# Optimization experiments

Hardware: AMD Instinct MI355X
Metric: run time of the kernel (lower is better)

Reference implementation:

```python
import jax, jax.numpy as jnp
import numpy as np

N_NODES = 50000
N_EDGES = 600000
DIM = 128
HEADS = 8
HEAD_DIM = DIM // HEADS  # 16


def leaky(x, slope=0.01):
    return jnp.where(x >= 0, x, slope * x)


def gat_layer(x, W, a_src, a_dst, bias, src, dst):
    # x: [N, DIM]; W: [DIM, DIM]; a_src/a_dst: [HEADS, HEAD_DIM]; bias: [DIM]
    N = x.shape[0]
    xh = (x @ W).reshape(N, HEADS, HEAD_DIM)
    alpha_src = jnp.sum(xh * a_src, axis=-1)  # [N, H]
    alpha_dst = jnp.sum(xh * a_dst, axis=-1)  # [N, H]
    e = leaky(alpha_src[src] + alpha_dst[dst], 0.2)  # [E, H], PyG negative_slope=0.2
    # segment softmax over edges sharing the same destination node
    e_max = jax.ops.segment_max(e, dst, num_segments=N)
    ex = jnp.exp(e - e_max[dst])
    denom = jax.ops.segment_sum(ex, dst, num_segments=N)
    alpha = ex / (denom[dst] + 1e-16)
    out = jax.ops.segment_sum(xh[src] * alpha[:, :, None], dst, num_segments=N)
    return out.reshape(N, DIM) + bias


def setup_inputs() -> dict:
    key = jax.random.key(0)
    ks = jax.random.split(key, 20)
    s_d = 1.0 / np.sqrt(DIM)
    s_h = 1.0 / np.sqrt(DIM // 2)
    inp = {
        'features': jax.random.normal(ks[0], (N_NODES, DIM), jnp.float32),
        'edge_index': jax.random.randint(ks[1], (2, N_EDGES), 0, N_NODES, jnp.int64)
            if jax.config.jax_enable_x64 else
            jax.random.randint(ks[1], (2, N_EDGES), 0, N_NODES).astype(jnp.int32),
        'W1': jax.random.normal(ks[2], (DIM, DIM), jnp.float32) * s_d,
        'a_src1': jax.random.normal(ks[3], (HEADS, HEAD_DIM), jnp.float32) * s_d,
        'a_dst1': jax.random.normal(ks[4], (HEADS, HEAD_DIM), jnp.float32) * s_d,
        'b1': jnp.zeros((DIM,), jnp.float32),
        'W2': jax.random.normal(ks[5], (DIM, DIM), jnp.float32) * s_d,
        'a_src2': jax.random.normal(ks[6], (HEADS, HEAD_DIM), jnp.float32) * s_d,
        'a_dst2': jax.random.normal(ks[7], (HEADS, HEAD_DIM), jnp.float32) * s_d,
        'b2': jnp.zeros((DIM,), jnp.float32),
        'wm1': jax.random.normal(ks[8], (DIM, DIM // 2), jnp.float32) * s_d,
        'bm1': jnp.zeros((DIM // 2,), jnp.float32),
        'wm2': jax.random.normal(ks[9], (DIM // 2, 1), jnp.float32) * s_h,
        'bm2': jnp.zeros((1,), jnp.float32),
        'wa1': jax.random.normal(ks[10], (DIM, DIM // 2), jnp.float32) * s_d,
        'ba1': jnp.zeros((DIM // 2,), jnp.float32),
        'wa2': jax.random.normal(ks[11], (DIM // 2, DIM), jnp.float32) * s_h,
        'ba2': jnp.zeros((DIM,), jnp.float32),
        'gamma': jnp.ones((DIM,), jnp.float32),
        'beta': jnp.zeros((DIM,), jnp.float32),
    }
    return inp


def reference(features, edge_index, W1, a_src1, a_dst1, b1, W2, a_src2, a_dst2, b2,
              wm1, bm1, wm2, bm2, wa1, ba1, wa2, ba2, gamma, beta):
    N = features.shape[0]
    loops = jnp.arange(N, dtype=edge_index.dtype)
    src = jnp.concatenate([edge_index[0], loops])  # PyG add_self_loops=True
    dst = jnp.concatenate([edge_index[1], loops])
    h = leaky(gat_layer(features, W1, a_src1, a_dst1, b1, src, dst))
    h = leaky(gat_layer(h, W2, a_src2, a_dst2, b2, src, dst))
    scores = (leaky(h @ wm1 + bm1) @ wm2 + bm2)[:, 0]  # [N]
    w = jax.nn.softmax(scores, axis=0)
    agg = jnp.sum(w[:, None] * h, axis=0)  # [DIM]
    z = leaky(agg @ wa1 + ba1) @ wa2 + ba2
    mu = jnp.mean(z)
    var = jnp.mean((z - mu) ** 2)
    return gamma * (z - mu) / jnp.sqrt(var + 1e-5) + beta
```

## Files before the change

kernel.cpp:

```cpp
#include <hip/hip_runtime.h>
#include <math.h>

#define DIM 128
#define HEADS 8
#define HD 16
#define CAP 64
#define WAGG_NB 512

typedef __attribute__((ext_vector_type(8))) short s16x8;
typedef __attribute__((ext_vector_type(8))) unsigned short u16x8;
typedef __attribute__((ext_vector_type(4))) float f32x4;

__device__ __forceinline__ float lrelu(float x, float s) { return x >= 0.f ? x : s * x; }

__device__ __forceinline__ unsigned short f2bf(float x) {
  unsigned u = __float_as_uint(x);
  return (unsigned short)((u + 0x7FFFu + ((u >> 16) & 1u)) >> 16);
}
__device__ __forceinline__ float bf2f(unsigned short b) {
  return __uint_as_float(((unsigned)b) << 16);
}

__global__ void k_hist(const int* __restrict__ ei, int E, int N, int* __restrict__ cnt) {
  int tot = E + N;
  for (int i = blockIdx.x * blockDim.x + threadIdx.x; i < tot; i += gridDim.x * blockDim.x) {
    int d = (i < E) ? ei[E + i] : (i - E);
    atomicAdd(&cnt[d], 1);
  }
}

__global__ __launch_bounds__(256) void k_scan_blk(const int* __restrict__ cnt, int n,
                                                  int* __restrict__ excl, int* __restrict__ bsum) {
  __shared__ int wsum[4];
  int tid = threadIdx.x, l = tid & 63, w = tid >> 6;
  int i = blockIdx.x * 256 + tid;
  int v = (i < n) ? cnt[i] : 0;
  int s = v;
#pragma unroll
  for (int off = 1; off < 64; off <<= 1) {
    int t = __shfl_up(s, off, 64);
    if (l >= off) s += t;
  }
  if (l == 63) wsum[w] = s;
  __syncthreads();
  int add = 0;
#pragma unroll
  for (int k = 0; k < 4; ++k) add += (k < w) ? wsum[k] : 0;
  if (i < n) excl[i] = s + add - v;
  if (tid == 255) bsum[blockIdx.x] = s + add;
}

__global__ __launch_bounds__(256) void k_scan_top(const int* __restrict__ bsum, int nb,
                                                  int* __restrict__ boff, int* __restrict__ rowptrN) {
  __shared__ int wsum[4];
  int tid = threadIdx.x, l = tid & 63, w = tid >> 6;
  int v = (tid < nb) ? bsum[tid] : 0;
  int s = v;
#pragma unroll
  for (int off = 1; off < 64; off <<= 1) {
    int t = __shfl_up(s, off, 64);
    if (l >= off) s += t;
  }
  if (l == 63) wsum[w] = s;
  __syncthreads();
  int add = 0;
#pragma unroll
  for (int k = 0; k < 4; ++k) add += (k < w) ? wsum[k] : 0;
  if (tid < nb) boff[tid] = s + add - v;
  if (tid == 255) *rowptrN = s + add;
}

__global__ __launch_bounds__(256) void k_scan_fix(int* __restrict__ cursor, const int* __restrict__ boff,
                                                  int n, int* __restrict__ rowptr) {
  int i = blockIdx.x * 256 + threadIdx.x;
  if (i < n) {
    int r = boff[blockIdx.x] + cursor[i];
    rowptr[i] = r;
    cursor[i] = r;
  }
}

__global__ void k_scatter(const int* __restrict__ ei, int E, int N,
                          int* __restrict__ cursor, int* __restrict__ colb) {
  int tot = E + N;
  for (int i = blockIdx.x * blockDim.x + threadIdx.x; i < tot; i += gridDim.x * blockDim.x) {
    int s, d;
    if (i < E) { s = ei[i]; d = ei[E + i]; } else { s = i - E; d = s; }
    int pos = atomicAdd(&cursor[d], 1);
    colb[pos] = s;
  }
}

__global__ __launch_bounds__(256) void k_prep(
    const float* __restrict__ W1, const float* __restrict__ as1, const float* __restrict__ ad1,
    const float* __restrict__ W2, const float* __restrict__ as2, const float* __restrict__ ad2,
    const float* __restrict__ wm1,
    unsigned short* __restrict__ wh1,
    unsigned short* __restrict__ sh1, unsigned short* __restrict__ sl1,
    unsigned short* __restrict__ wh2,
    unsigned short* __restrict__ sh2, unsigned short* __restrict__ sl2,
    unsigned short* __restrict__ mh, unsigned short* __restrict__ ml,
    int* __restrict__ cnt, int N) {
  int b = blockIdx.x, tid = threadIdx.x;
  if (b < 32) {
    int layer = b >> 4;
    const float* W = layer ? W2 : W1;
    unsigned short* wh = layer ? wh2 : wh1;
    int lo = (b & 15) * 1024;
    for (int idx = lo + tid; idx < lo + 1024; idx += 256) {
      int n = idx >> 7, k = idx & 127;
      wh[idx] = f2bf(W[k * DIM + n]);
    }
  } else if (b < 36) {
    int layer = (b - 32) >> 1;
    const float* W = layer ? W2 : W1;
    const float* avs = layer ? as2 : as1;
    const float* avd = layer ? ad2 : ad1;
    unsigned short* sh = layer ? sh2 : sh1;
    unsigned short* sl = layer ? sl2 : sl1;
    int lo = ((b - 32) & 1) * 1024;
    for (int idx = lo + tid; idx < lo + 1024; idx += 256) {
      int n = idx >> 7, k = idx & 127;
      float acc = 0.f;
      if (n < 8) {
#pragma unroll
        for (int j = 0; j < 16; ++j) acc += W[k * DIM + n * 16 + j] * avs[n * 16 + j];
      } else {
        int h = n - 8;
#pragma unroll
        for (int j = 0; j < 16; ++j) acc += W[k * DIM + h * 16 + j] * avd[h * 16 + j];
      }
      unsigned short hb = f2bf(acc);
      sh[idx] = hb;
      sl[idx] = f2bf(acc - bf2f(hb));
    }
  } else if (b < 44) {
    int lo = (b - 36) * 1024;
    for (int idx = lo + tid; idx < lo + 1024; idx += 256) {
      int j = idx >> 7, k = idx & 127;
      float v = wm1[k * 64 + j];
      unsigned short hb = f2bf(v);
      mh[idx] = hb;
      ml[idx] = f2bf(v - bf2f(hb));
    }
  } else {
    int i0 = (b - 44) * 2048 + tid * 8;
    if (i0 + 8 <= N) {
      int4 z = {0, 0, 0, 0};
      *(int4*)(cnt + i0) = z;
      *(int4*)(cnt + i0 + 4) = z;
    } else {
      for (int i = i0; i < N; ++i) cnt[i] = 0;
    }
  }
}

template <int BF16IN>
__global__ __launch_bounds__(256) void k_linear_mfma(
    const void* __restrict__ xin,
    const unsigned short* __restrict__ wh,
    const unsigned short* __restrict__ sh, const unsigned short* __restrict__ sl,
    unsigned short* __restrict__ xhb, float* __restrict__ asrc, float* __restrict__ adst,
    int N, int nrt) {
  int tid = threadIdx.x, l = tid & 63, w = tid >> 6;
  int g = l >> 4, c = l & 15;
  int t0 = w * 2, t1 = w * 2 + 1;

  const s16x8* Bh = (const s16x8*)wh;
  const s16x8* Shp = (const s16x8*)sh;
  const s16x8* Slp = (const s16x8*)sl;
  s16x8 B0[4], B1[4], S0[4], S1[4];
#pragma unroll
  for (int kt = 0; kt < 4; ++kt) {
    B0[kt] = Bh[(t0 * 16 + c) * 16 + kt * 4 + g];
    B1[kt] = Bh[(t1 * 16 + c) * 16 + kt * 4 + g];
    S0[kt] = Shp[c * 16 + kt * 4 + g];
    S1[kt] = Slp[c * 16 + kt * 4 + g];
  }

  for (int rt = blockIdx.x; rt < nrt; rt += gridDim.x) {
    int rbase = rt * 16;
    int rc = min(rbase + c, N - 1);
    s16x8 A[4];
    if constexpr (BF16IN) {
      const s16x8* xr = (const s16x8*)((const unsigned short*)xin + (size_t)rc * DIM);
#pragma unroll
      for (int kt = 0; kt < 4; ++kt) A[kt] = xr[kt * 4 + g];
    } else {
      const float4* xf = (const float4*)((const float*)xin + (size_t)rc * DIM);
#pragma unroll
      for (int kt = 0; kt < 4; ++kt) {
        float4 p = xf[kt * 8 + g * 2];
        float4 q = xf[kt * 8 + g * 2 + 1];
        s16x8 a;
        a[0] = (short)f2bf(p.x); a[1] = (short)f2bf(p.y);
        a[2] = (short)f2bf(p.z); a[3] = (short)f2bf(p.w);
        a[4] = (short)f2bf(q.x); a[5] = (short)f2bf(q.y);
        a[6] = (short)f2bf(q.z); a[7] = (short)f2bf(q.w);
        A[kt] = a;
      }
    }
    f32x4 acc0 = {0.f, 0.f, 0.f, 0.f}, acc1 = {0.f, 0.f, 0.f, 0.f};
#pragma unroll
    for (int kt = 0; kt < 4; ++kt) {
      acc0 = __builtin_amdgcn_mfma_f32_16x16x32_bf16(A[kt], B0[kt], acc0, 0, 0, 0);
      acc1 = __builtin_amdgcn_mfma_f32_16x16x32_bf16(A[kt], B1[kt], acc1, 0, 0, 0);
    }
#pragma unroll
    for (int r = 0; r < 4; ++r) {
      int rr = rbase + g * 4 + r;
      if (rr < N) {
        xhb[(size_t)rr * DIM + t0 * 16 + c] = f2bf(acc0[r]);
        xhb[(size_t)rr * DIM + t1 * 16 + c] = f2bf(acc1[r]);
      }
    }
    if (w == 0) {
      f32x4 accS = {0.f, 0.f, 0.f, 0.f};
#pragma unroll
      for (int kt = 0; kt < 4; ++kt) {
        accS = __builtin_amdgcn_mfma_f32_16x16x32_bf16(A[kt], S0[kt], accS, 0, 0, 0);
        accS = __builtin_amdgcn_mfma_f32_16x16x32_bf16(A[kt], S1[kt], accS, 0, 0, 0);
      }
#pragma unroll
      for (int r = 0; r < 4; ++r) {
        int rr = rbase + g * 4 + r;
        if (rr < N) {
          if (c < 8) asrc[rr * HEADS + c] = accS[r];
          else adst[rr * HEADS + (c - 8)] = accS[r];
        }
      }
    }
  }
}

__global__ __launch_bounds__(256) void k_gat_agg(const int* __restrict__ rowptr, const int* __restrict__ colb,
                                                 const unsigned short* __restrict__ xhb,
                                                 const float* __restrict__ asrc, const float* __restrict__ adst,
                                                 const float* __restrict__ bias,
                                                 unsigned short* __restrict__ houtb, int N) {
  __shared__ int ci[4][CAP];
  int tid = threadIdx.x, lane = tid & 63, wv = tid >> 6;
  int n = blockIdx.x * 4 + wv;
  int base = 0, deg = 0;
  if (n < N) { base = rowptr[n]; deg = rowptr[n + 1] - base; }
  if (lane < deg && lane < CAP) ci[wv][lane] = colb[base + lane];
  __syncthreads();
  if (n >= N) return;

  int qt = lane >> 4, q = lane & 15;
  int h = q >> 1;
  float adn = adst[n * HEADS + h];
  float den = 0.f;
  float a0 = 0.f, a1 = 0.f, a2 = 0.f, a3 = 0.f, a4 = 0.f, a5 = 0.f, a6 = 0.f, a7 = 0.f;
#define EDGE(ii) { \
    int c_ = ((ii) < CAP) ? ci[wv][(ii)] : colb[base + (ii)]; \
    float e_ = lrelu(asrc[c_ * HEADS + h] + adn, 0.2f); \
    float w_ = __expf(e_); \
    den += w_; \
    u16x8 u_ = *(const u16x8*)(xhb + (size_t)c_ * DIM + q * 8); \
    a0 = fmaf(w_, bf2f((unsigned short)u_[0]), a0); \
    a1 = fmaf(w_, bf2f((unsigned short)u_[1]), a1); \
    a2 = fmaf(w_, bf2f((unsigned short)u_[2]), a2); \
    a3 = fmaf(w_, bf2f((unsigned short)u_[3]), a3); \
    a4 = fmaf(w_, bf2f((unsigned short)u_[4]), a4); \
    a5 = fmaf(w_, bf2f((unsigned short)u_[5]), a5); \
    a6 = fmaf(w_, bf2f((unsigned short)u_[6]), a6); \
    a7 = fmaf(w_, bf2f((unsigned short)u_[7]), a7); }
  int i = qt;
  for (; i + 4 < deg; i += 8) { EDGE(i); EDGE(i + 4); }
  for (; i < deg; i += 4) { EDGE(i); }
#undef EDGE
  den += __shfl_xor(den, 16, 64); den += __shfl_xor(den, 32, 64);
  a0 += __shfl_xor(a0, 16, 64); a0 += __shfl_xor(a0, 32, 64);
  a1 += __shfl_xor(a1, 16, 64); a1 += __shfl_xor(a1, 32, 64);
  a2 += __shfl_xor(a2, 16, 64); a2 += __shfl_xor(a2, 32, 64);
  a3 += __shfl_xor(a3, 16, 64); a3 += __shfl_xor(a3, 32, 64);
  a4 += __shfl_xor(a4, 16, 64); a4 += __shfl_xor(a4, 32, 64);
  a5 += __shfl_xor(a5, 16, 64); a5 += __shfl_xor(a5, 32, 64);
  a6 += __shfl_xor(a6, 16, 64); a6 += __shfl_xor(a6, 32, 64);
  a7 += __shfl_xor(a7, 16, 64); a7 += __shfl_xor(a7, 32, 64);
  if (qt == 0) {
    float r = 1.f / (den + 1e-16f);
    const float4* bp = (const float4*)(bias + q * 8);
    float4 b0 = bp[0], b1 = bp[1];
    u16x8 o;
    o[0] = f2bf(lrelu(fmaf(a0, r, b0.x), 0.01f));
    o[1] = f2bf(lrelu(fmaf(a1, r, b0.y), 0.01f));
    o[2] = f2bf(lrelu(fmaf(a2, r, b0.z), 0.01f));
    o[3] = f2bf(lrelu(fmaf(a3, r, b0.w), 0.01f));
    o[4] = f2bf(lrelu(fmaf(a4, r, b1.x), 0.01f));
    o[5] = f2bf(lrelu(fmaf(a5, r, b1.y), 0.01f));
    o[6] = f2bf(lrelu(fmaf(a6, r, b1.z), 0.01f));
    o[7] = f2bf(lrelu(fmaf(a7, r, b1.w), 0.01f));
    *(u16x8*)(houtb + (size_t)n * DIM + q * 8) = o;
  }
}

__global__ __launch_bounds__(256) void k_score_mfma(
    const unsigned short* __restrict__ h2b,
    const unsigned short* __restrict__ mh, const unsigned short* __restrict__ ml,
    const float* __restrict__ bm1, const float* __restrict__ wm2, const float* __restrict__ bm2,
    float* __restrict__ scores, int N) {
  int tid = threadIdx.x, l = tid & 63, w = tid >> 6;
  int g = l >> 4, c = l & 15;
  int rbase = blockIdx.x * 64 + w * 16;
  int rc = min(rbase + c, N - 1);
  const s16x8* xr = (const s16x8*)(h2b + (size_t)rc * DIM);
  s16x8 A[4];
#pragma unroll
  for (int kt = 0; kt < 4; ++kt) A[kt] = xr[kt * 4 + g];

  const s16x8* Bh = (const s16x8*)mh;
  const s16x8* Bl = (const s16x8*)ml;
  float v[4] = {0.f, 0.f, 0.f, 0.f};
#pragma unroll
  for (int ct = 0; ct < 4; ++ct) {
    f32x4 acc = {0.f, 0.f, 0.f, 0.f};
#pragma unroll
    for (int kt = 0; kt < 4; ++kt) {
      s16x8 bh = Bh[(ct * 16 + c) * 16 + kt * 4 + g];
      s16x8 bl = Bl[(ct * 16 + c) * 16 + kt * 4 + g];
      acc = __builtin_amdgcn_mfma_f32_16x16x32_bf16(A[kt], bh, acc, 0, 0, 0);
      acc = __builtin_amdgcn_mfma_f32_16x16x32_bf16(A[kt], bl, acc, 0, 0, 0);
    }
    int col = ct * 16 + c;
    float b = bm1[col], w2 = wm2[col];
#pragma unroll
    for (int r = 0; r < 4; ++r) v[r] += lrelu(acc[r] + b, 0.01f) * w2;
  }
#pragma unroll
  for (int r = 0; r < 4; ++r) {
    v[r] += __shfl_xor(v[r], 1, 64);
    v[r] += __shfl_xor(v[r], 2, 64);
    v[r] += __shfl_xor(v[r], 4, 64);
    v[r] += __shfl_xor(v[r], 8, 64);
  }
  if (c == 0) {
    float b2 = bm2[0];
#pragma unroll
    for (int r = 0; r < 4; ++r) {
      int rr = rbase + g * 4 + r;
      if (rr < N) scores[rr] = v[r] + b2;
    }
  }
}

__global__ __launch_bounds__(128) void k_wagg(const float* __restrict__ scores,
                                              const unsigned short* __restrict__ h2b,
                                              int N, float* __restrict__ pagg, float* __restrict__ psum) {
  int d = threadIdx.x;
  float acc = 0.f, zs = 0.f;
  for (int n = blockIdx.x; n < N; n += gridDim.x) {
    float e = __expf(scores[n]);
    acc = fmaf(e, bf2f(h2b[(size_t)n * DIM + d]), acc);
    zs += e;
  }
  pagg[blockIdx.x * DIM + d] = acc;
  if (d == 0) psum[blockIdx.x] = zs;
}

__global__ __launch_bounds__(1024) void k_final(const float* __restrict__ psum, const float* __restrict__ pagg,
                                                int nb,
                                                const float* __restrict__ wa1, const float* __restrict__ ba1,
                                                const float* __restrict__ wa2, const float* __restrict__ ba2,
                                                const float* __restrict__ gamma, const float* __restrict__ beta,
                                                float* __restrict__ out) {
  __shared__ float redz[1024];
  __shared__ float reda[8][128];
  __shared__ float sa[128], shh[64], red[128];
  int t = threadIdx.x;
  float zp = 0.f;
  for (int b = t; b < nb; b += 1024) zp += psum[b];
  redz[t] = zp;
  __syncthreads();
  for (int st = 512; st > 0; st >>= 1) { if (t < st) redz[t] += redz[t + st]; __syncthreads(); }
  int d = t & 127, g = t >> 7;
  float ag = 0.f;
  for (int b = g; b < nb; b += 8) ag += pagg[b * DIM + d];
  reda[g][d] = ag;
  __syncthreads();
  if (g == 0) {
    float s = 0.f;
#pragma unroll
    for (int k = 0; k < 8; ++k) s += reda[k][d];
    sa[d] = s / redz[0];
  }
  __syncthreads();
  if (t < 64) {
    float a = 0.f;
    for (int k = 0; k < 128; ++k) a = fmaf(sa[k], wa1[k * 64 + t], a);
    a += ba1[t];
    shh[t] = lrelu(a, 0.01f);
  }
  __syncthreads();
  float zval = 0.f;
  if (t < 128) {
    zval = ba2[t];
    for (int j = 0; j < 64; ++j) zval = fmaf(shh[j], wa2[j * 128 + t], zval);
    red[t] = zval;
  }
  __syncthreads();
  for (int st = 64; st > 0; st >>= 1) { if (t < st) red[t] += red[t + st]; __syncthreads(); }
  float mu = red[0] / 128.f;
  __syncthreads();
  if (t < 128) red[t] = (zval - mu) * (zval - mu);
  __syncthreads();
  for (int st = 64; st > 0; st >>= 1) { if (t < st) red[t] += red[t + st]; __syncthreads(); }
  float var = red[0] / 128.f;
  if (t < 128) out[t] = gamma[t] * (zval - mu) / sqrtf(var + 1e-5f) + beta[t];
}

extern "C" void kernel_launch(void* const* d_in, const int* in_sizes, int n_in,
                              void* d_out, int out_size, void* d_ws, size_t ws_size,
                              hipStream_t stream) {
  const float* feat = (const float*)d_in[0];
  const int* ei = (const int*)d_in[1];
  const float* W1 = (const float*)d_in[2];
  const float* as1 = (const float*)d_in[3];
  const float* ad1 = (const float*)d_in[4];
  const float* b1 = (const float*)d_in[5];
  const float* W2 = (const float*)d_in[6];
  const float* as2 = (const float*)d_in[7];
  const float* ad2 = (const float*)d_in[8];
  const float* b2 = (const float*)d_in[9];
  const float* wm1 = (const float*)d_in[10];
  const float* bm1 = (const float*)d_in[11];
  const float* wm2 = (const float*)d_in[12];
  const float* bm2 = (const float*)d_in[13];
  const float* wa1 = (const float*)d_in[14];
  const float* ba1 = (const float*)d_in[15];
  const float* wa2 = (const float*)d_in[16];
  const float* ba2 = (const float*)d_in[17];
  const float* gamma = (const float*)d_in[18];
  const float* beta = (const float*)d_in[19];
  float* out = (float*)d_out;

  int N = in_sizes[0] / DIM;
  int E = in_sizes[1] / 2;
  int NB = (N + 255) / 256;
  int nrt = (N + 15) / 16;
  int ZB = (N + 2047) / 2048;

  char* ws = (char*)d_ws;
  size_t off = 0;
  auto alloc = [&](size_t bytes) -> void* {
    void* p = ws + off;
    off = (off + bytes + 255) & ~(size_t)255;
    return p;
  };
  int* cnt = (int*)alloc((size_t)N * 4);
  int* rowptr = (int*)alloc((size_t)(N + 1) * 4);
  int* cursor = (int*)alloc((size_t)N * 4);
  int* colb = (int*)alloc((size_t)(E + N) * 4);
  unsigned short* xhb = (unsigned short*)alloc((size_t)N * DIM * 2);
  unsigned short* h1b = (unsigned short*)alloc((size_t)N * DIM * 2);
  unsigned short* h2b = (unsigned short*)alloc((size_t)N * DIM * 2);
  float* asrcb = (float*)alloc((size_t)N * HEADS * 4);
  float* adstb = (float*)alloc((size_t)N * HEADS * 4);
  float* scores = (float*)alloc((size_t)N * 4);
  float* pagg = (float*)alloc((size_t)WAGG_NB * DIM * 4);
  float* psum = (float*)alloc((size_t)WAGG_NB * 4);
  int* bsum = (int*)alloc((size_t)NB * 4);
  int* boff = (int*)alloc((size_t)NB * 4);
  unsigned short* wh1 = (unsigned short*)alloc(DIM * DIM * 2);
  unsigned short* sh1 = (unsigned short*)alloc(16 * DIM * 2);
  unsigned short* sl1 = (unsigned short*)alloc(16 * DIM * 2);
  unsigned short* wh2 = (unsigned short*)alloc(DIM * DIM * 2);
  unsigned short* sh2 = (unsigned short*)alloc(16 * DIM * 2);
  unsigned short* sl2 = (unsigned short*)alloc(16 * DIM * 2);
  unsigned short* mh = (unsigned short*)alloc(64 * DIM * 2);
  unsigned short* ml = (unsigned short*)alloc(64 * DIM * 2);

  k_prep<<<44 + ZB, 256, 0, stream>>>(W1, as1, ad1, W2, as2, ad2, wm1,
                                      wh1, sh1, sl1, wh2, sh2, sl2, mh, ml, cnt, N);

  k_hist<<<1024, 256, 0, stream>>>(ei, E, N, cnt);
  k_scan_blk<<<NB, 256, 0, stream>>>(cnt, N, cursor, bsum);
  k_scan_top<<<1, 256, 0, stream>>>(bsum, NB, boff, rowptr + N);
  k_scan_fix<<<NB, 256, 0, stream>>>(cursor, boff, N, rowptr);
  k_scatter<<<1024, 256, 0, stream>>>(ei, E, N, cursor, colb);

  int gl = 1024;
  int gs = (N + 63) / 64;
  int ga = (N + 3) / 4;
  k_linear_mfma<0><<<gl, 256, 0, stream>>>(feat, wh1, sh1, sl1, xhb, asrcb, adstb, N, nrt);
  k_gat_agg<<<ga, 256, 0, stream>>>(rowptr, colb, xhb, asrcb, adstb, b1, h1b, N);
  k_linear_mfma<1><<<gl, 256, 0, stream>>>(h1b, wh2, sh2, sl2, xhb, asrcb, adstb, N, nrt);
  k_gat_agg<<<ga, 256, 0, stream>>>(rowptr, colb, xhb, asrcb, adstb, b2, h2b, N);

  k_score_mfma<<<gs, 256, 0, stream>>>(h2b, mh, ml, bm1, wm2, bm2, scores, N);
  k_wagg<<<WAGG_NB, 128, 0, stream>>>(scores, h2b, N, pagg, psum);
  k_final<<<1, 1024, 0, stream>>>(psum, pagg, WAGG_NB, wa1, ba1, wa2, ba2, gamma, beta, out);
}
```

Measured before the change: 256.7 us.

## Fuse edge histogram into first linear kernel and pooling into score kernel

The degree histogram now runs as extra blocks appended to the first linear MFMA launch, so the atomics overlap with the matmul instead of occupying their own launch. The score kernel now also computes exp(score)-weighted feature sums and partition sums from the row tiles it already holds in registers, which removes the separate k_wagg pass that reread h2 and the intermediate scores buffer. In exchange, k_final has to reduce about 782 partial rows instead of 512. The unnormalized exp without a max shift is kept from the earlier code.

```diff
diff --git a/kernel.cpp b/kernel.cpp
--- a/kernel.cpp
+++ b/kernel.cpp
@@ -5,7 +5,6 @@
 #define HEADS 8
 #define HD 16
 #define CAP 64
-#define WAGG_NB 512
 
 typedef __attribute__((ext_vector_type(8))) short s16x8;
 typedef __attribute__((ext_vector_type(8))) unsigned short u16x8;
@@ -19,14 +18,6 @@
 }
 __device__ __forceinline__ float bf2f(unsigned short b) {
   return __uint_as_float(((unsigned)b) << 16);
-}
-
-__global__ void k_hist(const int* __restrict__ ei, int E, int N, int* __restrict__ cnt) {
-  int tot = E + N;
-  for (int i = blockIdx.x * blockDim.x + threadIdx.x; i < tot; i += gridDim.x * blockDim.x) {
-    int d = (i < E) ? ei[E + i] : (i - E);
-    atomicAdd(&cnt[d], 1);
-  }
 }
 
 __global__ __launch_bounds__(256) void k_scan_blk(const int* __restrict__ cnt, int n,
@@ -155,16 +146,29 @@
   }
 }
 
-template <int BF16IN>
+template <int BF16IN, int FUSEHIST>
 __global__ __launch_bounds__(256) void k_linear_mfma(
     const void* __restrict__ xin,
     const unsigned short* __restrict__ wh,
     const unsigned short* __restrict__ sh, const unsigned short* __restrict__ sl,
     unsigned short* __restrict__ xhb, float* __restrict__ asrc, float* __restrict__ adst,
-    int N, int nrt) {
+    int N, int nrt, int GL,
+    const int* __restrict__ ei, int E, int* __restrict__ cnt) {
+  if constexpr (FUSEHIST) {
+    if ((int)blockIdx.x >= GL) {
+      int tot = E + N;
+      int nhb = gridDim.x - GL;
+      for (int i = ((int)blockIdx.x - GL) * 256 + (int)threadIdx.x; i < tot; i += nhb * 256) {
+        int d = (i < E) ? ei[E + i] : (i - E);
+        atomicAdd(&cnt[d], 1);
+      }
+      return;
+    }
+  }
   int tid = threadIdx.x, l = tid & 63, w = tid >> 6;
   int g = l >> 4, c = l & 15;
   int t0 = w * 2, t1 = w * 2 + 1;
+  int stride = FUSEHIST ? GL : (int)gridDim.x;
 
   const s16x8* Bh = (const s16x8*)wh;
   const s16x8* Shp = (const s16x8*)sh;
@@ -178,7 +182,7 @@
     S1[kt] = Slp[c * 16 + kt * 4 + g];
   }
 
-  for (int rt = blockIdx.x; rt < nrt; rt += gridDim.x) {
+  for (int rt = blockIdx.x; rt < nrt; rt += stride) {
     int rbase = rt * 16;
     int rc = min(rbase + c, N - 1);
     s16x8 A[4];
@@ -296,11 +300,14 @@
   }
 }
 
-__global__ __launch_bounds__(256) void k_score_mfma(
+__global__ __launch_bounds__(256) void k_score_pool(
     const unsigned short* __restrict__ h2b,
     const unsigned short* __restrict__ mh, const unsigned short* __restrict__ ml,
     const float* __restrict__ bm1, const float* __restrict__ wm2, const float* __restrict__ bm2,
-    float* __restrict__ scores, int N) {
+    float* __restrict__ pagg, float* __restrict__ psum, int N) {
+  __shared__ float se[4][16];
+  __shared__ float blkacc[4][128];
+  __shared__ float swave[4];
   int tid = threadIdx.x, l = tid & 63, w = tid >> 6;
   int g = l >> 4, c = l & 15;
   int rbase = blockIdx.x * 64 + w * 16;
@@ -335,28 +342,49 @@
     v[r] += __shfl_xor(v[r], 4, 64);
     v[r] += __shfl_xor(v[r], 8, 64);
   }
+  float b2 = bm2[0];
+  float e[4];
+#pragma unroll
+  for (int r = 0; r < 4; ++r) {
+    int rr = rbase + g * 4 + r;
+    e[r] = (rr < N) ? __expf(v[r] + b2) : 0.f;
+  }
   if (c == 0) {
-    float b2 = bm2[0];
-#pragma unroll
-    for (int r = 0; r < 4; ++r) {
-      int rr = rbase + g * 4 + r;
-      if (rr < N) scores[rr] = v[r] + b2;
-    }
-  }
-}
-
-__global__ __launch_bounds__(128) void k_wagg(const float* __restrict__ scores,
-                                              const unsigned short* __restrict__ h2b,
-                                              int N, float* __restrict__ pagg, float* __restrict__ psum) {
-  int d = threadIdx.x;
-  float acc = 0.f, zs = 0.f;
-  for (int n = blockIdx.x; n < N; n += gridDim.x) {
-    float e = __expf(scores[n]);
-    acc = fmaf(e, bf2f(h2b[(size_t)n * DIM + d]), acc);
-    zs += e;
-  }
-  pagg[blockIdx.x * DIM + d] = acc;
-  if (d == 0) psum[blockIdx.x] = zs;
+#pragma unroll
+    for (int r = 0; r < 4; ++r) se[w][g * 4 + r] = e[r];
+  }
+  __syncthreads();
+  float emy = se[w][c];
+  float pa[32];
+#pragma unroll
+  for (int kt = 0; kt < 4; ++kt)
+#pragma unroll
+    for (int j = 0; j < 8; ++j)
+      pa[kt * 8 + j] = emy * bf2f((unsigned short)A[kt][j]);
+#pragma unroll
+  for (int k = 0; k < 32; ++k) {
+    pa[k] += __shfl_xor(pa[k], 1, 64);
+    pa[k] += __shfl_xor(pa[k], 2, 64);
+    pa[k] += __shfl_xor(pa[k], 4, 64);
+    pa[k] += __shfl_xor(pa[k], 8, 64);
+  }
+  if (c == 0) {
+#pragma unroll
+    for (int kt = 0; kt < 4; ++kt)
+#pragma unroll
+      for (int j = 0; j < 8; ++j)
+        blkacc[w][kt * 32 + g * 8 + j] = pa[kt * 8 + j];
+  }
+  float ws = e[0] + e[1] + e[2] + e[3];
+  ws += __shfl_xor(ws, 16, 64);
+  ws += __shfl_xor(ws, 32, 64);
+  if (l == 0) swave[w] = ws;
+  __syncthreads();
+  if (tid < 128) {
+    float s = blkacc[0][tid] + blkacc[1][tid] + blkacc[2][tid] + blkacc[3][tid];
+    pagg[(size_t)blockIdx.x * DIM + tid] = s;
+  }
+  if (tid == 0) psum[blockIdx.x] = swave[0] + swave[1] + swave[2] + swave[3];
 }
 
 __global__ __launch_bounds__(1024) void k_final(const float* __restrict__ psum, const float* __restrict__ pagg,
@@ -376,7 +404,7 @@
   for (int st = 512; st > 0; st >>= 1) { if (t < st) redz[t] += redz[t + st]; __syncthreads(); }
   int d = t & 127, g = t >> 7;
   float ag = 0.f;
-  for (int b = g; b < nb; b += 8) ag += pagg[b * DIM + d];
+  for (int b = g; b < nb; b += 8) ag += pagg[(size_t)b * DIM + d];
   reda[g][d] = ag;
   __syncthreads();
   if (g == 0) {
@@ -440,6 +468,9 @@
   int NB = (N + 255) / 256;
   int nrt = (N + 15) / 16;
   int ZB = (N + 2047) / 2048;
+  int GL = 1024;
+  int GH = 512;
+  int gs = (N + 63) / 64;
 
   char* ws = (char*)d_ws;
   size_t off = 0;
@@ -457,9 +488,8 @@
   unsigned short* h2b = (unsigned short*)alloc((size_t)N * DIM * 2);
   float* asrcb = (float*)alloc((size_t)N * HEADS * 4);
   float* adstb = (float*)alloc((size_t)N * HEADS * 4);
-  float* scores = (float*)alloc((size_t)N * 4);
-  float* pagg = (float*)alloc((size_t)WAGG_NB * DIM * 4);
-  float* psum = (float*)alloc((size_t)WAGG_NB * 4);
+  float* pagg = (float*)alloc((size_t)gs * DIM * 4);
+  float* psum = (float*)alloc((size_t)gs * 4);
   int* bsum = (int*)alloc((size_t)NB * 4);
   int* boff = (int*)alloc((size_t)NB * 4);
   unsigned short* wh1 = (unsigned short*)alloc(DIM * DIM * 2);
@@ -474,21 +504,20 @@
   k_prep<<<44 + ZB, 256, 0, stream>>>(W1, as1, ad1, W2, as2, ad2, wm1,
                                       wh1, sh1, sl1, wh2, sh2, sl2, mh, ml, cnt, N);
 
-  k_hist<<<1024, 256, 0, stream>>>(ei, E, N, cnt);
+  k_linear_mfma<0, 1><<<GL + GH, 256, 0, stream>>>(feat, wh1, sh1, sl1, xhb, asrcb, adstb,
+                                                   N, nrt, GL, ei, E, cnt);
+
   k_scan_blk<<<NB, 256, 0, stream>>>(cnt, N, cursor, bsum);
   k_scan_top<<<1, 256, 0, stream>>>(bsum, NB, boff, rowptr + N);
   k_scan_fix<<<NB, 256, 0, stream>>>(cursor, boff, N, rowptr);
   k_scatter<<<1024, 256, 0, stream>>>(ei, E, N, cursor, colb);
 
-  int gl = 1024;
-  int gs = (N + 63) / 64;
   int ga = (N + 3) / 4;
-  k_linear_mfma<0><<<gl, 256, 0, stream>>>(feat, wh1, sh1, sl1, xhb, asrcb, adstb, N, nrt);
   k_gat_agg<<<ga, 256, 0, stream>>>(rowptr, colb, xhb, asrcb, adstb, b1, h1b, N);
-  k_linear_mfma<1><<<gl, 256, 0, stream>>>(h1b, wh2, sh2, sl2, xhb, asrcb, adstb, N, nrt);
+  k_linear_mfma<1, 0><<<1024, 256, 0, stream>>>(h1b, wh2, sh2, sl2, xhb, asrcb, adstb,
+                                                N, nrt, 0, nullptr, 0, nullptr);
   k_gat_agg<<<ga, 256, 0, stream>>>(rowptr, colb, xhb, asrcb, adstb, b2, h2b, N);
 
-  k_score_mfma<<<gs, 256, 0, stream>>>(h2b, mh, ml, bm1, wm2, bm2, scores, N);
-  k_wagg<<<WAGG_NB, 128, 0, stream>>>(scores, h2b, N, pagg, psum);
-  k_final<<<1, 1024, 0, stream>>>(psum, pagg, WAGG_NB, wa1, ba1, wa2, ba2, gamma, beta, out);
-}
+  k_score_pool<<<gs, 256, 0, stream>>>(h2b, mh, ml, bm1, wm2, bm2, pagg, psum, N);
+  k_final<<<1, 1024, 0, stream>>>(psum, pagg, gs, wa1, ba1, wa2, ba2, gamma, beta, out);
+}
```

Result: faster. 235.0 us (-8.4%).
